# Kernel tuning notes

Hardware: AMD Instinct MI355X
Metric: run time of the kernel (lower is better)

## Reference

```python
import jax, jax.numpy as jnp
import numpy as np

EPS = 1e-5

def layer_norm(x, w, b):
    mu = jnp.mean(x, axis=-1, keepdims=True)
    var = jnp.mean(jnp.square(x - mu), axis=-1, keepdims=True)
    return (x - mu) * jax.lax.rsqrt(var + EPS) * w + b

def setup_inputs() -> dict:
    key = jax.random.key(0)
    ks = jax.random.split(key, 10)
    B, S, E = 8, 1024, 512
    s = 1.0 / np.sqrt(E)
    return {
        "Zi_1_alpha_beta": jax.random.normal(ks[0], (B, S, E), jnp.float32),
        "Zi_1_alpha": jax.random.normal(ks[1], (B, S, E), jnp.float32),
        "ln_w": jnp.ones((E,), jnp.float32),
        "ln_b": jnp.zeros((E,), jnp.float32),
        "in_proj_w": jax.random.uniform(ks[2], (3 * E, E), jnp.float32, -s, s),
        "in_proj_b": jnp.zeros((3 * E,), jnp.float32),
        "out_proj_w": jax.random.uniform(ks[3], (E, E), jnp.float32, -s, s),
        "out_proj_b": jnp.zeros((E,), jnp.float32),
        "ff_w": jax.random.uniform(ks[4], (E, E), jnp.float32, -s, s),
        "ff_b": jax.random.uniform(ks[5], (E,), jnp.float32, -s, s),
    }

def reference(Zi_1_alpha_beta, Zi_1_alpha, ln_w, ln_b, in_proj_w, in_proj_b,
              out_proj_w, out_proj_b, ff_w, ff_b):
    B, Sq, E = Zi_1_alpha_beta.shape
    Sk = Zi_1_alpha.shape[1]
    H = 8
    dh = E // H

    q_in = layer_norm(Zi_1_alpha_beta, ln_w, ln_b)   # query source
    kv_in = layer_norm(Zi_1_alpha, ln_w, ln_b)       # key/value source

    Wq, Wk, Wv = in_proj_w[:E], in_proj_w[E:2 * E], in_proj_w[2 * E:]
    bq, bk, bv = in_proj_b[:E], in_proj_b[E:2 * E], in_proj_b[2 * E:]
    q = (q_in @ Wq.T + bq).reshape(B, Sq, H, dh)
    k = (kv_in @ Wk.T + bk).reshape(B, Sk, H, dh)
    v = (kv_in @ Wv.T + bv).reshape(B, Sk, H, dh)

    scale = 1.0 / np.sqrt(dh)
    scores = jnp.einsum('bqhd,bkhd->bhqk', q, k) * scale   # [B,H,Sq,Sk]
    attn = jax.nn.softmax(scores, axis=-1)
    ctx = jnp.einsum('bhqk,bkhd->bqhd', attn, v).reshape(B, Sq, E)
    attn_out = ctx @ out_proj_w.T + out_proj_b

    # torch MHA with need_weights=True averages weights over heads
    attn_weights = jnp.mean(attn, axis=1)  # [B,Sq,Sk]

    x = attn_out + Zi_1_alpha_beta
    x_n = layer_norm(x, ln_w, ln_b)
    ff = x_n @ ff_w.T + ff_b
    final = layer_norm(x_n + ff, ln_w, ln_b)
    return final, attn_weights
```

## Files before the change

kernel.cpp:

```cpp
#include <hip/hip_runtime.h>
#include <math.h>

#define EPS 1e-5f

constexpr int B = 8, S = 1024, E = 512, H = 8;
constexpr int M = B * S;

typedef __attribute__((ext_vector_type(8))) short short8;
typedef __attribute__((ext_vector_type(4))) float f32x4;

static __device__ __forceinline__ unsigned short f2bf(float f) {
    unsigned int x = __float_as_uint(f);
    x += 0x7FFFu + ((x >> 16) & 1u);
    return (unsigned short)(x >> 16);
}
static __device__ __forceinline__ float bf2f(unsigned short u) {
    return __uint_as_float(((unsigned int)u) << 16);
}

typedef __attribute__((address_space(3))) unsigned int  lds_uint;
typedef __attribute__((address_space(1))) unsigned int  glb_uint;
static __device__ __forceinline__ void gload16(const unsigned short* g, unsigned short* l) {
    __builtin_amdgcn_global_load_lds((const glb_uint*)g, (lds_uint*)l, 16, 0, 0);
}
template <int N>
static __device__ __forceinline__ void waitvm() {
    __builtin_amdgcn_s_waitcnt(0x0F70 | N);
}

__global__ __launch_bounds__(256) void ln_bf16_kernel(
    const float* __restrict__ x, const float* __restrict__ w,
    const float* __restrict__ bb, unsigned short* __restrict__ out) {
    int row = blockIdx.x * 4 + (threadIdx.x >> 6);
    int lane = threadIdx.x & 63;
    const float* xr = x + (size_t)row * E + lane * 8;
    float4 v0 = *(const float4*)xr;
    float4 v1 = *(const float4*)(xr + 4);
    float vv[8] = {v0.x, v0.y, v0.z, v0.w, v1.x, v1.y, v1.z, v1.w};
    float s = 0.f;
    #pragma unroll
    for (int i = 0; i < 8; i++) s += vv[i];
    #pragma unroll
    for (int o = 1; o < 64; o <<= 1) s += __shfl_xor(s, o);
    float mu = s * (1.0f / E);
    float qs = 0.f;
    #pragma unroll
    for (int i = 0; i < 8; i++) { float d = vv[i] - mu; qs += d * d; }
    #pragma unroll
    for (int o = 1; o < 64; o <<= 1) qs += __shfl_xor(qs, o);
    float rs = rsqrtf(qs * (1.0f / E) + EPS);
    float4 w0 = *(const float4*)(w + lane * 8), w1 = *(const float4*)(w + lane * 8 + 4);
    float4 b0 = *(const float4*)(bb + lane * 8), b1 = *(const float4*)(bb + lane * 8 + 4);
    float ww[8] = {w0.x, w0.y, w0.z, w0.w, w1.x, w1.y, w1.z, w1.w};
    float bv[8] = {b0.x, b0.y, b0.z, b0.w, b1.x, b1.y, b1.z, b1.w};
    short8 o8;
    #pragma unroll
    for (int i = 0; i < 8; i++) o8[i] = (short)f2bf((vv[i] - mu) * rs * ww[i] + bv[i]);
    *(short8*)(out + (size_t)row * E + lane * 8) = o8;
}

__global__ __launch_bounds__(256) void ln_full_kernel(
    const float* __restrict__ x, const float* __restrict__ w,
    const float* __restrict__ bb, float* __restrict__ out) {
    int row = blockIdx.x * 4 + (threadIdx.x >> 6);
    int lane = threadIdx.x & 63;
    const float* xr = x + (size_t)row * E + lane * 8;
    float4 v0 = *(const float4*)xr;
    float4 v1 = *(const float4*)(xr + 4);
    float vv[8] = {v0.x, v0.y, v0.z, v0.w, v1.x, v1.y, v1.z, v1.w};
    float s = 0.f;
    #pragma unroll
    for (int i = 0; i < 8; i++) s += vv[i];
    #pragma unroll
    for (int o = 1; o < 64; o <<= 1) s += __shfl_xor(s, o);
    float mu = s * (1.0f / E);
    float qs = 0.f;
    #pragma unroll
    for (int i = 0; i < 8; i++) { float d = vv[i] - mu; qs += d * d; }
    #pragma unroll
    for (int o = 1; o < 64; o <<= 1) qs += __shfl_xor(qs, o);
    float rs = rsqrtf(qs * (1.0f / E) + EPS);
    float4 w0 = *(const float4*)(w + lane * 8), w1 = *(const float4*)(w + lane * 8 + 4);
    float4 b0 = *(const float4*)(bb + lane * 8), b1 = *(const float4*)(bb + lane * 8 + 4);
    float* op = out + (size_t)row * E + lane * 8;
    float4 o0, o1;
    o0.x = (vv[0] - mu) * rs * w0.x + b0.x;
    o0.y = (vv[1] - mu) * rs * w0.y + b0.y;
    o0.z = (vv[2] - mu) * rs * w0.z + b0.z;
    o0.w = (vv[3] - mu) * rs * w0.w + b0.w;
    o1.x = (vv[4] - mu) * rs * w1.x + b1.x;
    o1.y = (vv[5] - mu) * rs * w1.y + b1.y;
    o1.z = (vv[6] - mu) * rs * w1.z + b1.z;
    o1.w = (vv[7] - mu) * rs * w1.w + b1.w;
    *(float4*)op = o0;
    *(float4*)(op + 4) = o1;
}

__global__ __launch_bounds__(256) void w2bf_kernel(
    const float* __restrict__ wqkv, const float* __restrict__ wo,
    const float* __restrict__ wf, unsigned short* __restrict__ out) {
    int base = (blockIdx.x * 256 + threadIdx.x) * 4;
    float4 v;
    if (base < 3 * E * E)           v = *(const float4*)(wqkv + base);
    else if (base < 4 * E * E)      v = *(const float4*)(wo + (base - 3 * E * E));
    else                            v = *(const float4*)(wf + (base - 4 * E * E));
    ushort4 o;
    o.x = f2bf(v.x); o.y = f2bf(v.y); o.z = f2bf(v.z); o.w = f2bf(v.w);
    *(ushort4*)(out + base) = o;
}

template <int OUT_MODE>
__global__ __launch_bounds__(256) void gemm_mfma(
    const unsigned short* __restrict__ A, const unsigned short* __restrict__ W,
    const float* __restrict__ bias,
    const float* __restrict__ residf, const unsigned short* __restrict__ residb,
    void* __restrict__ C0, void* __restrict__ C1, int Ntot) {
    __shared__ unsigned short As[128 * 32];
    __shared__ unsigned short Bs[128 * 32];
    const int t = threadIdx.x;
    const int wave = t >> 6, lane = t & 63;
    const int quad = lane >> 4, l16 = lane & 15;
    const int m0 = blockIdx.x * 128, n0 = blockIdx.y * 128;
    const int wm = (wave >> 1) * 64, wn = (wave & 1) * 64;

    const int srow = t >> 2;
    const int skof = (t & 3) * 8;

    f32x4 acc[4][4];
    #pragma unroll
    for (int i = 0; i < 4; i++)
        #pragma unroll
        for (int j = 0; j < 4; j++) acc[i][j] = (f32x4){0.f, 0.f, 0.f, 0.f};

    for (int k0 = 0; k0 < E; k0 += 32) {
        gload16(A + (size_t)(m0 + srow) * E + k0 + skof,        As + t * 8);
        gload16(A + (size_t)(m0 + 64 + srow) * E + k0 + skof,   As + 2048 + t * 8);
        gload16(W + (size_t)(n0 + srow) * E + k0 + skof,        Bs + t * 8);
        gload16(W + (size_t)(n0 + 64 + srow) * E + k0 + skof,   Bs + 2048 + t * 8);
        __syncthreads();
        short8 af[4], bfr[4];
        #pragma unroll
        for (int i = 0; i < 4; i++)
            af[i] = *(const short8*)&As[(wm + i * 16 + l16) * 32 + quad * 8];
        #pragma unroll
        for (int j = 0; j < 4; j++)
            bfr[j] = *(const short8*)&Bs[(wn + j * 16 + l16) * 32 + quad * 8];
        #pragma unroll
        for (int i = 0; i < 4; i++)
            #pragma unroll
            for (int j = 0; j < 4; j++)
                acc[i][j] = __builtin_amdgcn_mfma_f32_16x16x32_bf16(af[i], bfr[j], acc[i][j], 0, 0, 0);
        __syncthreads();
    }

    #pragma unroll
    for (int i = 0; i < 4; i++) {
        const int mrow0 = m0 + wm + i * 16 + quad * 4;
        #pragma unroll
        for (int j = 0; j < 4; j++) {
            const int ncol = n0 + wn + j * 16 + l16;
            const float bval = bias[ncol];
            if (OUT_MODE == 0) {
                #pragma unroll
                for (int r = 0; r < 4; r++)
                    ((unsigned short*)C0)[(size_t)(mrow0 + r) * Ntot + ncol] =
                        f2bf(acc[i][j][r] + bval);
            } else if (OUT_MODE == 1) {
                #pragma unroll
                for (int r = 0; r < 4; r++) {
                    size_t idx = (size_t)(mrow0 + r) * Ntot + ncol;
                    ((float*)C0)[idx] = acc[i][j][r] + bval + residf[idx];
                }
            } else if (OUT_MODE == 2) {
                #pragma unroll
                for (int r = 0; r < 4; r++) {
                    size_t idx = (size_t)(mrow0 + r) * Ntot + ncol;
                    ((float*)C0)[idx] = acc[i][j][r] + bval + bf2f(residb[idx]);
                }
            } else {
                if (ncol < 512) {
                    #pragma unroll
                    for (int r = 0; r < 4; r++)
                        ((unsigned short*)C0)[(size_t)(mrow0 + r) * 512 + ncol] =
                            f2bf(acc[i][j][r] + bval);
                } else {
                    const int nv = ncol - 512;
                    const int b2 = mrow0 >> 10, s0v = mrow0 & 1023;
                    ushort4 o;
                    o.x = f2bf(acc[i][j][0] + bval);
                    o.y = f2bf(acc[i][j][1] + bval);
                    o.z = f2bf(acc[i][j][2] + bval);
                    o.w = f2bf(acc[i][j][3] + bval);
                    *(ushort4*)((unsigned short*)C1 + ((size_t)b2 * 512 + nv) * 1024 + s0v) = o;
                }
            }
        }
    }
}

__global__ __launch_bounds__(256, 2) void attn_mfma_kernel(
    const unsigned short* __restrict__ q,
    const unsigned short* __restrict__ k,
    const unsigned short* __restrict__ vt,
    unsigned short* __restrict__ ctx,
    unsigned short* __restrict__ awp) {
    __shared__ unsigned short s_mem[16 * 1032];
    __shared__ unsigned short s_v[4 * 2048];
    __shared__ float s_red[2][4][16];

    const int t = threadIdx.x;
    const int wave = t >> 6, lane = t & 63;
    const int quad = lane >> 4, l16 = lane & 15;
    const int qt   = blockIdx.x & 63;
    const int rest = blockIdx.x >> 6;
    const int hg   = rest & 3;
    const int b    = rest >> 2;
    const int q0   = qt * 16;
    const size_t qrow = ((size_t)(b * S + q0 + l16)) * E;

    unsigned short* karea = s_mem + wave * 4128;
    unsigned short* varea = s_v + wave * 2048;

    const int dr = lane >> 3;
    const int dc = lane & 7;
    const int csrc = dc ^ dr;
    const int sw7 = l16 & 7;

    f32x4 awacc[16];
    #pragma unroll
    for (int i = 0; i < 16; i++) awacc[i] = (f32x4){0.f, 0.f, 0.f, 0.f};

    for (int hh = 0; hh < 2; hh++) {
        const int h = hg * 2 + hh;

        auto stage_k = [&](int c, int buf) {
            const unsigned short* src =
                k + ((size_t)(b * S + wave * 256 + c * 32 + dr)) * E + h * 64 + csrc * 8;
            unsigned short* dst = karea + buf * 2048 + dr * 64 + dc * 8;
            gload16(src,                  dst);
            gload16(src + (size_t)8 * E,  dst + 512);
            gload16(src + (size_t)16 * E, dst + 1024);
            gload16(src + (size_t)24 * E, dst + 1536);
        };
        auto stage_v = [&](int cv, int buf) {
            const unsigned short* src =
                vt + ((size_t)(b * E + h * 64 + wave * 16 + dr)) * S + cv * 64 + csrc * 8;
            unsigned short* dst = varea + buf * 1024 + dr * 64 + dc * 8;
            gload16(src,                 dst);
            gload16(src + (size_t)8 * S, dst + 512);
        };

        short8 aq0 = *(const short8*)(q + qrow + h * 64 + quad * 8);
        short8 aq1 = *(const short8*)(q + qrow + h * 64 + 32 + quad * 8);

        f32x4 sacc[16];
        stage_k(0, 0);
        stage_k(1, 1);
        #pragma unroll
        for (int c = 0; c < 8; c++) {
            if (c < 7) waitvm<4>(); else waitvm<0>();
            const unsigned short* kbuf = karea + (c & 1) * 2048;
            #pragma unroll
            for (int ntl = 0; ntl < 2; ntl++) {
                const int rl = ntl * 16 + l16;
                short8 kf0 = *(const short8*)(kbuf + rl * 64 + ((quad)     ^ sw7) * 8);
                short8 kf1 = *(const short8*)(kbuf + rl * 64 + ((4 + quad) ^ sw7) * 8);
                f32x4 cc = (f32x4){0.f, 0.f, 0.f, 0.f};
                cc = __builtin_amdgcn_mfma_f32_16x16x32_bf16(aq0, kf0, cc, 0, 0, 0);
                cc = __builtin_amdgcn_mfma_f32_16x16x32_bf16(aq1, kf1, cc, 0, 0, 0);
                sacc[c * 2 + ntl] = cc * 0.125f;
            }
            if (c < 6) stage_k(c + 2, c & 1);
        }

        float lm[4], ls[4];
        #pragma unroll
        for (int r = 0; r < 4; r++) {
            float mv = sacc[0][r];
            #pragma unroll
            for (int nt = 1; nt < 16; nt++) mv = fmaxf(mv, sacc[nt][r]);
            #pragma unroll
            for (int o = 1; o < 16; o <<= 1) mv = fmaxf(mv, __shfl_xor(mv, o));
            lm[r] = mv;
            ls[r] = 0.f;
        }
        #pragma unroll
        for (int nt = 0; nt < 16; nt++)
            #pragma unroll
            for (int r = 0; r < 4; r++) {
                float e = __expf(sacc[nt][r] - lm[r]);
                sacc[nt][r] = e;
                ls[r] += e;
            }
        #pragma unroll
        for (int r = 0; r < 4; r++) {
            #pragma unroll
            for (int o = 1; o < 16; o <<= 1) ls[r] += __shfl_xor(ls[r], o);
        }
        if (l16 == 0) {
            #pragma unroll
            for (int r = 0; r < 4; r++) {
                s_red[0][wave][quad * 4 + r] = lm[r];
                s_red[1][wave][quad * 4 + r] = ls[r];
            }
        }
        __syncthreads();
        float scale[4];
        #pragma unroll
        for (int r = 0; r < 4; r++) {
            const int row = quad * 4 + r;
            float m0 = s_red[0][0][row], m1 = s_red[0][1][row];
            float m2 = s_red[0][2][row], m3 = s_red[0][3][row];
            float gmax = fmaxf(fmaxf(m0, m1), fmaxf(m2, m3));
            float gsum = s_red[1][0][row] * __expf(m0 - gmax)
                       + s_red[1][1][row] * __expf(m1 - gmax)
                       + s_red[1][2][row] * __expf(m2 - gmax)
                       + s_red[1][3][row] * __expf(m3 - gmax);
            scale[r] = __expf(lm[r] - gmax) / gsum;
        }

        #pragma unroll
        for (int nt = 0; nt < 16; nt++) {
            #pragma unroll
            for (int r = 0; r < 4; r++) {
                float p = sacc[nt][r] * scale[r];
                awacc[nt][r] += p;
                s_mem[(quad * 4 + r) * 1032 + wave * 256 + nt * 16 + l16] = f2bf(p);
            }
        }
        __syncthreads();

        f32x4 cacc0 = (f32x4){0.f, 0.f, 0.f, 0.f};
        f32x4 cacc1 = (f32x4){0.f, 0.f, 0.f, 0.f};
        stage_v(0, 0);
        stage_v(1, 1);
        #pragma unroll
        for (int cv = 0; cv < 16; cv++) {
            if (cv < 15) waitvm<2>(); else waitvm<0>();
            const unsigned short* vbuf = varea + (cv & 1) * 1024;
            short8 vf0 = *(const short8*)(vbuf + l16 * 64 + ((quad)     ^ sw7) * 8);
            short8 vf1 = *(const short8*)(vbuf + l16 * 64 + ((4 + quad) ^ sw7) * 8);
            short8 pf0 = *(const short8*)(s_mem + l16 * 1032 + cv * 64 + quad * 8);
            short8 pf1 = *(const short8*)(s_mem + l16 * 1032 + cv * 64 + 32 + quad * 8);
            cacc0 = __builtin_amdgcn_mfma_f32_16x16x32_bf16(pf0, vf0, cacc0, 0, 0, 0);
            cacc1 = __builtin_amdgcn_mfma_f32_16x16x32_bf16(pf1, vf1, cacc1, 0, 0, 0);
            if (cv < 14) stage_v(cv + 2, cv & 1);
        }
        f32x4 cacc = cacc0 + cacc1;
        unsigned short* crow = ctx + ((size_t)(b * S + q0)) * E + h * 64 + wave * 16 + l16;
        #pragma unroll
        for (int r = 0; r < 4; r++)
            crow[(size_t)(quad * 4 + r) * E] = f2bf(cacc[r]);
        __syncthreads();
    }

    #pragma unroll
    for (int nt = 0; nt < 16; nt++) {
        #pragma unroll
        for (int r = 0; r < 4; r++)
            awp[((size_t)((hg * B + b) * S + q0 + quad * 4 + r)) * S +
                wave * 256 + nt * 16 + l16] = f2bf(awacc[nt][r]);
    }
}

template <int NP>
__global__ __launch_bounds__(256) void aw_reduce_kernel(
    const unsigned short* __restrict__ awp, float* __restrict__ aw) {
    const size_t PLN = (size_t)B * S * S;
    size_t idx = ((size_t)blockIdx.x * 256 + threadIdx.x) * 8;
    float acc[8] = {};
    #pragma unroll
    for (int p = 0; p < NP; p++) {
        short8 v = *(const short8*)(awp + p * PLN + idx);
        #pragma unroll
        for (int j = 0; j < 8; j++) acc[j] += bf2f((unsigned short)v[j]);
    }
    float4 o0 = make_float4(acc[0] * (1.0f / H), acc[1] * (1.0f / H),
                            acc[2] * (1.0f / H), acc[3] * (1.0f / H));
    float4 o1 = make_float4(acc[4] * (1.0f / H), acc[5] * (1.0f / H),
                            acc[6] * (1.0f / H), acc[7] * (1.0f / H));
    *(float4*)(aw + idx) = o0;
    *(float4*)(aw + idx + 4) = o1;
}

extern "C" void kernel_launch(void* const* d_in, const int* in_sizes, int n_in,
                              void* d_out, int out_size, void* d_ws, size_t ws_size,
                              hipStream_t stream) {
    const float* Zab  = (const float*)d_in[0];
    const float* Za   = (const float*)d_in[1];
    const float* lnw  = (const float*)d_in[2];
    const float* lnb  = (const float*)d_in[3];
    const float* Wqkv = (const float*)d_in[4];
    const float* bqkv = (const float*)d_in[5];
    const float* Wo   = (const float*)d_in[6];
    const float* bo   = (const float*)d_in[7];
    const float* Wf   = (const float*)d_in[8];
    const float* bf   = (const float*)d_in[9];

    float* out_final = (float*)d_out;
    float* out_aw    = out_final + (size_t)B * S * E;

    char* ws = (char*)d_ws;
    unsigned short* qb   = (unsigned short*)(ws);
    unsigned short* kb   = (unsigned short*)(ws + (8u << 20));
    unsigned short* vtb  = (unsigned short*)(ws + (16u << 20));
    unsigned short* ctxb = (unsigned short*)(ws + (24u << 20));
    unsigned short* aqb  = (unsigned short*)(ws + (32u << 20));
    unsigned short* akvb = (unsigned short*)(ws + (40u << 20));
    unsigned short* awp  = (unsigned short*)(ws + (32ull << 20));
    unsigned short* wbf  = (unsigned short*)(ws + (96ull << 20));
    float* xb  = (float*)(ws);
    float* tb  = (float*)(ws + (16u << 20));
    unsigned short* xnb = aqb;

    dim3 blk(256);

    w2bf_kernel<<<(5 * E * E) / 1024, blk, 0, stream>>>(Wqkv, Wo, Wf, wbf);

    ln_bf16_kernel<<<M / 4, blk, 0, stream>>>(Zab, lnw, lnb, aqb);
    ln_bf16_kernel<<<M / 4, blk, 0, stream>>>(Za,  lnw, lnb, akvb);

    gemm_mfma<0><<<dim3(M / 128, 4), blk, 0, stream>>>(aqb,  wbf,               bqkv,     nullptr, nullptr, qb, nullptr, 512);
    gemm_mfma<3><<<dim3(M / 128, 8), blk, 0, stream>>>(akvb, wbf + (size_t)E*E, bqkv + E, nullptr, nullptr, kb, vtb, 1024);

    attn_mfma_kernel<<<B * 4 * 64, blk, 0, stream>>>(qb, kb, vtb, ctxb, awp);
    aw_reduce_kernel<4><<<4096, blk, 0, stream>>>(awp, out_aw);

    gemm_mfma<1><<<dim3(M / 128, 4), blk, 0, stream>>>(ctxb, wbf + (size_t)3*E*E, bo, Zab, nullptr, xb, nullptr, 512);

    ln_bf16_kernel<<<M / 4, blk, 0, stream>>>(xb, lnw, lnb, xnb);

    gemm_mfma<2><<<dim3(M / 128, 4), blk, 0, stream>>>(xnb, wbf + (size_t)4*E*E, bf, nullptr, xnb, tb, nullptr, 512);

    ln_full_kernel<<<M / 4, blk, 0, stream>>>(tb, lnw, lnb, out_final);
}
```

Before: 283.9 us.

## Loop all heads per attention block and write averaged weights directly

The attention kernel now processes all 8 heads in one block, so each block covers one batch and one 16-query tile, and it writes the head-averaged fp32 attention weights directly. This removes the partial bf16 weight planes and the separate reduction kernel along with their global traffic. K and V are now read from global memory straight into registers with a 4-deep software prefetch, replacing the LDS staging through global_load_lds. The trade-off is a grid of only 512 blocks, one quarter of the previous count, with longer serial work per block, which may leave the GPU underoccupied.

```diff
diff --git a/kernel.cpp b/kernel.cpp
--- a/kernel.cpp
+++ b/kernel.cpp
@@ -22,10 +22,6 @@
 typedef __attribute__((address_space(1))) unsigned int  glb_uint;
 static __device__ __forceinline__ void gload16(const unsigned short* g, unsigned short* l) {
     __builtin_amdgcn_global_load_lds((const glb_uint*)g, (lds_uint*)l, 16, 0, 0);
-}
-template <int N>
-static __device__ __forceinline__ void waitvm() {
-    __builtin_amdgcn_s_waitcnt(0x0F70 | N);
 }
 
 __global__ __launch_bounds__(256) void ln_bf16_kernel(
@@ -203,74 +199,46 @@
     const unsigned short* __restrict__ k,
     const unsigned short* __restrict__ vt,
     unsigned short* __restrict__ ctx,
-    unsigned short* __restrict__ awp) {
-    __shared__ unsigned short s_mem[16 * 1032];
-    __shared__ unsigned short s_v[4 * 2048];
+    float* __restrict__ aw) {
+    __shared__ unsigned short s_p[16 * 1032];
     __shared__ float s_red[2][4][16];
 
     const int t = threadIdx.x;
     const int wave = t >> 6, lane = t & 63;
     const int quad = lane >> 4, l16 = lane & 15;
-    const int qt   = blockIdx.x & 63;
-    const int rest = blockIdx.x >> 6;
-    const int hg   = rest & 3;
-    const int b    = rest >> 2;
-    const int q0   = qt * 16;
+    const int b  = blockIdx.x & 7;
+    const int qt = blockIdx.x >> 3;
+    const int q0 = qt * 16;
     const size_t qrow = ((size_t)(b * S + q0 + l16)) * E;
 
-    unsigned short* karea = s_mem + wave * 4128;
-    unsigned short* varea = s_v + wave * 2048;
-
-    const int dr = lane >> 3;
-    const int dc = lane & 7;
-    const int csrc = dc ^ dr;
-    const int sw7 = l16 & 7;
-
     f32x4 awacc[16];
     #pragma unroll
     for (int i = 0; i < 16; i++) awacc[i] = (f32x4){0.f, 0.f, 0.f, 0.f};
 
-    for (int hh = 0; hh < 2; hh++) {
-        const int h = hg * 2 + hh;
-
-        auto stage_k = [&](int c, int buf) {
-            const unsigned short* src =
-                k + ((size_t)(b * S + wave * 256 + c * 32 + dr)) * E + h * 64 + csrc * 8;
-            unsigned short* dst = karea + buf * 2048 + dr * 64 + dc * 8;
-            gload16(src,                  dst);
-            gload16(src + (size_t)8 * E,  dst + 512);
-            gload16(src + (size_t)16 * E, dst + 1024);
-            gload16(src + (size_t)24 * E, dst + 1536);
-        };
-        auto stage_v = [&](int cv, int buf) {
-            const unsigned short* src =
-                vt + ((size_t)(b * E + h * 64 + wave * 16 + dr)) * S + cv * 64 + csrc * 8;
-            unsigned short* dst = varea + buf * 1024 + dr * 64 + dc * 8;
-            gload16(src,                 dst);
-            gload16(src + (size_t)8 * S, dst + 512);
-        };
-
+    #pragma clang loop unroll(disable)
+    for (int h = 0; h < H; h++) {
         short8 aq0 = *(const short8*)(q + qrow + h * 64 + quad * 8);
         short8 aq1 = *(const short8*)(q + qrow + h * 64 + 32 + quad * 8);
 
+        const unsigned short* kbase =
+            k + ((size_t)(b * S + wave * 256 + l16)) * E + h * 64 + quad * 8;
         f32x4 sacc[16];
-        stage_k(0, 0);
-        stage_k(1, 1);
-        #pragma unroll
-        for (int c = 0; c < 8; c++) {
-            if (c < 7) waitvm<4>(); else waitvm<0>();
-            const unsigned short* kbuf = karea + (c & 1) * 2048;
-            #pragma unroll
-            for (int ntl = 0; ntl < 2; ntl++) {
-                const int rl = ntl * 16 + l16;
-                short8 kf0 = *(const short8*)(kbuf + rl * 64 + ((quad)     ^ sw7) * 8);
-                short8 kf1 = *(const short8*)(kbuf + rl * 64 + ((4 + quad) ^ sw7) * 8);
-                f32x4 cc = (f32x4){0.f, 0.f, 0.f, 0.f};
-                cc = __builtin_amdgcn_mfma_f32_16x16x32_bf16(aq0, kf0, cc, 0, 0, 0);
-                cc = __builtin_amdgcn_mfma_f32_16x16x32_bf16(aq1, kf1, cc, 0, 0, 0);
-                sacc[c * 2 + ntl] = cc * 0.125f;
-            }
-            if (c < 6) stage_k(c + 2, c & 1);
+        short8 ka[4], kb1[4];
+        #pragma unroll
+        for (int g = 0; g < 4; g++) {
+            ka[g]  = *(const short8*)(kbase + (size_t)g * 16 * E);
+            kb1[g] = *(const short8*)(kbase + (size_t)g * 16 * E + 32);
+        }
+        #pragma unroll
+        for (int g = 0; g < 16; g++) {
+            f32x4 cc = (f32x4){0.f, 0.f, 0.f, 0.f};
+            cc = __builtin_amdgcn_mfma_f32_16x16x32_bf16(aq0, ka[g & 3], cc, 0, 0, 0);
+            cc = __builtin_amdgcn_mfma_f32_16x16x32_bf16(aq1, kb1[g & 3], cc, 0, 0, 0);
+            sacc[g] = cc * 0.125f;
+            if (g < 12) {
+                ka[g & 3]  = *(const short8*)(kbase + (size_t)(g + 4) * 16 * E);
+                kb1[g & 3] = *(const short8*)(kbase + (size_t)(g + 4) * 16 * E + 32);
+            }
         }
 
         float lm[4], ls[4];
@@ -325,26 +293,31 @@
             for (int r = 0; r < 4; r++) {
                 float p = sacc[nt][r] * scale[r];
                 awacc[nt][r] += p;
-                s_mem[(quad * 4 + r) * 1032 + wave * 256 + nt * 16 + l16] = f2bf(p);
-            }
-        }
-        __syncthreads();
-
+                s_p[(quad * 4 + r) * 1032 + wave * 256 + nt * 16 + l16] = f2bf(p);
+            }
+        }
+        __syncthreads();
+
+        const unsigned short* vbase =
+            vt + ((size_t)(b * E + h * 64 + wave * 16 + l16)) * S + quad * 8;
         f32x4 cacc0 = (f32x4){0.f, 0.f, 0.f, 0.f};
         f32x4 cacc1 = (f32x4){0.f, 0.f, 0.f, 0.f};
-        stage_v(0, 0);
-        stage_v(1, 1);
+        short8 va[4], vb[4];
+        #pragma unroll
+        for (int cv = 0; cv < 4; cv++) {
+            va[cv] = *(const short8*)(vbase + cv * 64);
+            vb[cv] = *(const short8*)(vbase + cv * 64 + 32);
+        }
         #pragma unroll
         for (int cv = 0; cv < 16; cv++) {
-            if (cv < 15) waitvm<2>(); else waitvm<0>();
-            const unsigned short* vbuf = varea + (cv & 1) * 1024;
-            short8 vf0 = *(const short8*)(vbuf + l16 * 64 + ((quad)     ^ sw7) * 8);
-            short8 vf1 = *(const short8*)(vbuf + l16 * 64 + ((4 + quad) ^ sw7) * 8);
-            short8 pf0 = *(const short8*)(s_mem + l16 * 1032 + cv * 64 + quad * 8);
-            short8 pf1 = *(const short8*)(s_mem + l16 * 1032 + cv * 64 + 32 + quad * 8);
-            cacc0 = __builtin_amdgcn_mfma_f32_16x16x32_bf16(pf0, vf0, cacc0, 0, 0, 0);
-            cacc1 = __builtin_amdgcn_mfma_f32_16x16x32_bf16(pf1, vf1, cacc1, 0, 0, 0);
-            if (cv < 14) stage_v(cv + 2, cv & 1);
+            short8 pf0 = *(const short8*)(s_p + l16 * 1032 + cv * 64 + quad * 8);
+            short8 pf1 = *(const short8*)(s_p + l16 * 1032 + cv * 64 + 32 + quad * 8);
+            cacc0 = __builtin_amdgcn_mfma_f32_16x16x32_bf16(pf0, va[cv & 3], cacc0, 0, 0, 0);
+            cacc1 = __builtin_amdgcn_mfma_f32_16x16x32_bf16(pf1, vb[cv & 3], cacc1, 0, 0, 0);
+            if (cv < 12) {
+                va[cv & 3] = *(const short8*)(vbase + (cv + 4) * 64);
+                vb[cv & 3] = *(const short8*)(vbase + (cv + 4) * 64 + 32);
+            }
         }
         f32x4 cacc = cacc0 + cacc1;
         unsigned short* crow = ctx + ((size_t)(b * S + q0)) * E + h * 64 + wave * 16 + l16;
@@ -358,29 +331,9 @@
     for (int nt = 0; nt < 16; nt++) {
         #pragma unroll
         for (int r = 0; r < 4; r++)
-            awp[((size_t)((hg * B + b) * S + q0 + quad * 4 + r)) * S +
-                wave * 256 + nt * 16 + l16] = f2bf(awacc[nt][r]);
+            aw[((size_t)(b * S + q0 + quad * 4 + r)) * S +
+               wave * 256 + nt * 16 + l16] = awacc[nt][r] * (1.0f / H);
     }
-}
-
-template <int NP>
-__global__ __launch_bounds__(256) void aw_reduce_kernel(
-    const unsigned short* __restrict__ awp, float* __restrict__ aw) {
-    const size_t PLN = (size_t)B * S * S;
-    size_t idx = ((size_t)blockIdx.x * 256 + threadIdx.x) * 8;
-    float acc[8] = {};
-    #pragma unroll
-    for (int p = 0; p < NP; p++) {
-        short8 v = *(const short8*)(awp + p * PLN + idx);
-        #pragma unroll
-        for (int j = 0; j < 8; j++) acc[j] += bf2f((unsigned short)v[j]);
-    }
-    float4 o0 = make_float4(acc[0] * (1.0f / H), acc[1] * (1.0f / H),
-                            acc[2] * (1.0f / H), acc[3] * (1.0f / H));
-    float4 o1 = make_float4(acc[4] * (1.0f / H), acc[5] * (1.0f / H),
-                            acc[6] * (1.0f / H), acc[7] * (1.0f / H));
-    *(float4*)(aw + idx) = o0;
-    *(float4*)(aw + idx + 4) = o1;
 }
 
 extern "C" void kernel_launch(void* const* d_in, const int* in_sizes, int n_in,
@@ -407,7 +360,6 @@
     unsigned short* ctxb = (unsigned short*)(ws + (24u << 20));
     unsigned short* aqb  = (unsigned short*)(ws + (32u << 20));
     unsigned short* akvb = (unsigned short*)(ws + (40u << 20));
-    unsigned short* awp  = (unsigned short*)(ws + (32ull << 20));
     unsigned short* wbf  = (unsigned short*)(ws + (96ull << 20));
     float* xb  = (float*)(ws);
     float* tb  = (float*)(ws + (16u << 20));
@@ -423,8 +375,7 @@
     gemm_mfma<0><<<dim3(M / 128, 4), blk, 0, stream>>>(aqb,  wbf,               bqkv,     nullptr, nullptr, qb, nullptr, 512);
     gemm_mfma<3><<<dim3(M / 128, 8), blk, 0, stream>>>(akvb, wbf + (size_t)E*E, bqkv + E, nullptr, nullptr, kb, vtb, 1024);
 
-    attn_mfma_kernel<<<B * 4 * 64, blk, 0, stream>>>(qb, kb, vtb, ctxb, awp);
-    aw_reduce_kernel<4><<<4096, blk, 0, stream>>>(awp, out_aw);
+    attn_mfma_kernel<<<B * 64, blk, 0, stream>>>(qb, kb, vtb, ctxb, out_aw);
 
     gemm_mfma<1><<<dim3(M / 128, 4), blk, 0, stream>>>(ctxb, wbf + (size_t)3*E*E, bo, Zab, nullptr, xb, nullptr, 512);
 
```

New measurement: 318.3 us. 12.1% more time.
